# Performance work log

Measured on AMD Instinct MI355X. Metric: run time of the kernel, lower is better.

Reference implementation:

```python
import jax, jax.numpy as jnp
import numpy as np
import math

B, S, T = 8, 512, 512
D, H, DFF = 512, 8, 2048
LE, LD = 4, 4
DK = D // H
NEG = -1e9
EPS = 1e-5


def _posenc(L, d):
    pos = jnp.arange(L, dtype=jnp.float32)[:, None]
    div = jnp.exp(jnp.arange(0, d, 2, dtype=jnp.float32) * (-math.log(10000.0) / d))
    pe = jnp.zeros((L, d), jnp.float32)
    pe = pe.at[:, 0::2].set(jnp.sin(pos * div))
    pe = pe.at[:, 1::2].set(jnp.cos(pos * div))
    return pe  # [L, d]


def _layernorm(x, g, b):
    mu = jnp.mean(x, axis=-1, keepdims=True)
    var = jnp.mean(jnp.square(x - mu), axis=-1, keepdims=True)
    return (x - mu) * jax.lax.rsqrt(var + EPS) * g + b


def _mha(xq, xkv, W, b, mask):
    # W: [4, D, D] (q,k,v,o); b: [4, D]
    Bq, Lq, _ = xq.shape
    Lk = xkv.shape[1]
    q = (xq @ W[0] + b[0]).reshape(Bq, Lq, H, DK).transpose(0, 2, 1, 3)
    k = (xkv @ W[1] + b[1]).reshape(Bq, Lk, H, DK).transpose(0, 2, 1, 3)
    v = (xkv @ W[2] + b[2]).reshape(Bq, Lk, H, DK).transpose(0, 2, 1, 3)
    scores = jnp.einsum('bhqd,bhkd->bhqk', q, k) / math.sqrt(DK)
    if mask is not None:
        scores = jnp.where(mask, scores, NEG)
    attn = jax.nn.softmax(scores, axis=-1)
    o = jnp.einsum('bhqk,bhkd->bhqd', attn, v).transpose(0, 2, 1, 3).reshape(Bq, Lq, D)
    return o @ W[3] + b[3]


def _ffn(x, W1, b1, W2, b2):
    return jax.nn.relu(x @ W1 + b1) @ W2 + b2


def setup_inputs() -> dict:
    key = jax.random.key(0)
    ks = iter(jax.random.split(key, 32))
    w = lambda shape: jax.random.normal(next(ks), shape, jnp.float32) * 0.02
    inp = {
        'src': jax.random.normal(next(ks), (B, S, D), jnp.float32),
        'tgt': jax.random.normal(next(ks), (B, T, D), jnp.float32),
        'enc_attn_W': w((LE, 4, D, D)), 'enc_attn_b': jnp.zeros((LE, 4, D)),
        'enc_ffn_W1': w((LE, D, DFF)), 'enc_ffn_b1': jnp.zeros((LE, DFF)),
        'enc_ffn_W2': w((LE, DFF, D)), 'enc_ffn_b2': jnp.zeros((LE, D)),
        'enc_ln_g': jnp.ones((LE, 2, D)), 'enc_ln_b': jnp.zeros((LE, 2, D)),
        'enc_fnorm_g': jnp.ones((D,)), 'enc_fnorm_b': jnp.zeros((D,)),
        'dec_sattn_W': w((LD, 4, D, D)), 'dec_sattn_b': jnp.zeros((LD, 4, D)),
        'dec_cattn_W': w((LD, 4, D, D)), 'dec_cattn_b': jnp.zeros((LD, 4, D)),
        'dec_ffn_W1': w((LD, D, DFF)), 'dec_ffn_b1': jnp.zeros((LD, DFF)),
        'dec_ffn_W2': w((LD, DFF, D)), 'dec_ffn_b2': jnp.zeros((LD, D)),
        'dec_ln_g': jnp.ones((LD, 3, D)), 'dec_ln_b': jnp.zeros((LD, 3, D)),
        'dec_fnorm_g': jnp.ones((D,)), 'dec_fnorm_b': jnp.zeros((D,)),
        'tgt_mask': jnp.tril(jnp.ones((T, T), bool))[None, None],  # [1,1,T,T] causal
    }
    return inp


def reference(src, tgt, enc_attn_W, enc_attn_b, enc_ffn_W1, enc_ffn_b1,
              enc_ffn_W2, enc_ffn_b2, enc_ln_g, enc_ln_b, enc_fnorm_g, enc_fnorm_b,
              dec_sattn_W, dec_sattn_b, dec_cattn_W, dec_cattn_b,
              dec_ffn_W1, dec_ffn_b1, dec_ffn_W2, dec_ffn_b2,
              dec_ln_g, dec_ln_b, dec_fnorm_g, dec_fnorm_b, tgt_mask):
    # positional encoding (dropout = identity in eval)
    x = src + _posenc(S, D)[None]
    y = tgt + _posenc(T, D)[None]

    # ----- encoder -----
    for l in range(LE):
        a = _mha(x, x, enc_attn_W[l], enc_attn_b[l], None)
        x = _layernorm(x + a, enc_ln_g[l, 0], enc_ln_b[l, 0])
        f = _ffn(x, enc_ffn_W1[l], enc_ffn_b1[l], enc_ffn_W2[l], enc_ffn_b2[l])
        x = _layernorm(x + f, enc_ln_g[l, 1], enc_ln_b[l, 1])
    memory = _layernorm(x, enc_fnorm_g, enc_fnorm_b)

    # ----- decoder -----
    for l in range(LD):
        a = _mha(y, y, dec_sattn_W[l], dec_sattn_b[l], tgt_mask)
        y = _layernorm(y + a, dec_ln_g[l, 0], dec_ln_b[l, 0])
        c = _mha(y, memory, dec_cattn_W[l], dec_cattn_b[l], None)
        y = _layernorm(y + c, dec_ln_g[l, 1], dec_ln_b[l, 1])
        f = _ffn(y, dec_ffn_W1[l], dec_ffn_b1[l], dec_ffn_W2[l], dec_ffn_b2[l])
        y = _layernorm(y + f, dec_ln_g[l, 2], dec_ln_b[l, 2])
    out = _layernorm(y, dec_fnorm_g, dec_fnorm_b)
    return out
```

## Files before the change

kernel.cpp:

```cpp
#include <hip/hip_runtime.h>

typedef _Float16 half_t;
typedef _Float16 f16x8 __attribute__((ext_vector_type(8)));
typedef _Float16 f16x4 __attribute__((ext_vector_type(4)));
typedef float    f32x4 __attribute__((ext_vector_type(4)));

#define MFMA16(a, b, c) __builtin_amdgcn_mfma_f32_16x16x32_f16((a), (b), (c), 0, 0, 0)

#define BB   8
#define SS   512
#define DD   512
#define HH   8
#define DFFN 2048
#define MTOT 4096
#define MMAT 262144L
#define FFMAT 1048576L
#define ACTST 2097152L

__device__ __forceinline__ void gload16(const half_t* g, half_t* l) {
    __builtin_amdgcn_global_load_lds((const __attribute__((address_space(1))) void*)g,
                                     (__attribute__((address_space(3))) void*)l, 16, 0, 0);
}

__global__ __launch_bounds__(256) void wtrans(const float* __restrict__ W,
                                              half_t* __restrict__ Wt, int K, int N) {
    const long z = blockIdx.z;
    W += z * (long)K * N;
    Wt += z * (long)K * N;
    __shared__ float t[32][33];
    const int n0 = blockIdx.x * 32, k0 = blockIdx.y * 32;
    const int tx = threadIdx.x, ty = threadIdx.y;
#pragma unroll
    for (int i = 0; i < 4; i++)
        t[ty + i * 8][tx] = W[(long)(k0 + ty + i * 8) * N + n0 + tx];
    __syncthreads();
#pragma unroll
    for (int i = 0; i < 4; i++)
        Wt[(long)(n0 + ty + i * 8) * K + k0 + tx] = (half_t)t[tx][ty + i * 8];
}

__global__ __launch_bounds__(256) void vtrans(const half_t* __restrict__ V,
                                              half_t* __restrict__ Vt, int Lk) {
    const int z = blockIdx.z, b = z >> 3, h = z & 7;
    const int s0 = blockIdx.x * 32, d0 = blockIdx.y * 32;
    const int tx = threadIdx.x, ty = threadIdx.y;
    __shared__ half_t t[32][33];
#pragma unroll
    for (int i = 0; i < 4; i++)
        t[ty + i * 8][tx] = V[(long)(b * Lk + s0 + ty + i * 8) * DD + h * 64 + d0 + tx];
    __syncthreads();
#pragma unroll
    for (int i = 0; i < 4; i++)
        Vt[(long)(z * 64 + d0 + ty + i * 8) * Lk + s0 + tx] = t[tx][ty + i * 8];
}

__global__ __launch_bounds__(256) void vtransc(const half_t* __restrict__ ckv,
                                               half_t* __restrict__ vtc) {
    const int zz = blockIdx.z, l = zz >> 6, z = zz & 63, b = z >> 3, h = z & 7;
    const half_t* V = ckv + (long)(2 * l + 1) * ACTST;
    half_t* Vt = vtc + (long)l * ACTST;
    const int s0 = blockIdx.x * 32, d0 = blockIdx.y * 32;
    const int tx = threadIdx.x, ty = threadIdx.y;
    __shared__ half_t t[32][33];
#pragma unroll
    for (int i = 0; i < 4; i++)
        t[ty + i * 8][tx] = V[(long)(b * SS + s0 + ty + i * 8) * DD + h * 64 + d0 + tx];
    __syncthreads();
#pragma unroll
    for (int i = 0; i < 4; i++)
        Vt[(long)(z * 64 + d0 + ty + i * 8) * SS + s0 + tx] = t[tx][ty + i * 8];
}

__global__ __launch_bounds__(256) void posenc_k(const float* __restrict__ src,
                                                half_t* __restrict__ out) {
    const int idx = blockIdx.x * 256 + threadIdx.x;
    const long f = (long)idx * 4;
    const int d0 = (int)(f & 511);
    const int srow = (int)((f >> 9) & 511);
    float4 v = *(const float4*)(src + f);
    const float cexp = -0.0359778926f;
    const int p0 = d0 >> 1;
    const float a0 = (float)srow * __expf(cexp * (float)p0);
    const float a1 = (float)srow * __expf(cexp * (float)(p0 + 1));
    v.x += __sinf(a0);
    v.y += __cosf(a0);
    v.z += __sinf(a1);
    v.w += __cosf(a1);
    f16x4 h;
    h[0] = (half_t)v.x; h[1] = (half_t)v.y; h[2] = (half_t)v.z; h[3] = (half_t)v.w;
    *(f16x4*)(out + f) = h;
}

template <int HASRES, int F32OUT>
__global__ __launch_bounds__(256) void ln_k(const half_t* __restrict__ X,
                                            const half_t* __restrict__ R,
                                            const float* __restrict__ gam,
                                            const float* __restrict__ bet,
                                            void* __restrict__ out) {
    const int wid = threadIdx.x >> 6, lane = threadIdx.x & 63;
    const long row = blockIdx.x * 4 + wid;
    const int c = lane * 8;
    float v[8];
    f16x8 xv = *(const f16x8*)(X + row * 512 + c);
    if (HASRES) {
        f16x8 rv = *(const f16x8*)(R + row * 512 + c);
#pragma unroll
        for (int i = 0; i < 8; i++) v[i] = (float)xv[i] + (float)rv[i];
    } else {
#pragma unroll
        for (int i = 0; i < 8; i++) v[i] = (float)xv[i];
    }
    float s = 0.f, sq = 0.f;
#pragma unroll
    for (int i = 0; i < 8; i++) { s += v[i]; sq += v[i] * v[i]; }
#pragma unroll
    for (int m = 1; m < 64; m <<= 1) {
        s += __shfl_xor(s, m);
        sq += __shfl_xor(sq, m);
    }
    const float mu = s * (1.f / 512.f);
    const float var = sq * (1.f / 512.f) - mu * mu;
    const float rstd = rsqrtf(var + 1e-5f);
    float4 g0 = *(const float4*)(gam + c), g1 = *(const float4*)(gam + c + 4);
    float4 b0 = *(const float4*)(bet + c), b1 = *(const float4*)(bet + c + 4);
    float gg[8] = {g0.x, g0.y, g0.z, g0.w, g1.x, g1.y, g1.z, g1.w};
    float bb[8] = {b0.x, b0.y, b0.z, b0.w, b1.x, b1.y, b1.z, b1.w};
    if (F32OUT) {
        float* o = (float*)out + row * 512 + c;
        float4 o0, o1;
        o0.x = (v[0] - mu) * rstd * gg[0] + bb[0];
        o0.y = (v[1] - mu) * rstd * gg[1] + bb[1];
        o0.z = (v[2] - mu) * rstd * gg[2] + bb[2];
        o0.w = (v[3] - mu) * rstd * gg[3] + bb[3];
        o1.x = (v[4] - mu) * rstd * gg[4] + bb[4];
        o1.y = (v[5] - mu) * rstd * gg[5] + bb[5];
        o1.z = (v[6] - mu) * rstd * gg[6] + bb[6];
        o1.w = (v[7] - mu) * rstd * gg[7] + bb[7];
        *(float4*)o = o0;
        *(float4*)(o + 4) = o1;
    } else {
        f16x8 hv;
#pragma unroll
        for (int i = 0; i < 8; i++) hv[i] = (half_t)((v[i] - mu) * rstd * gg[i] + bb[i]);
        *(f16x8*)((half_t*)out + row * 512 + c) = hv;
    }
}

template <int MR, int RELU, int ZMAP>
__global__ __launch_bounds__(256) void gemm_k(const half_t* __restrict__ A,
                                              const half_t* __restrict__ Wt,
                                              const float* __restrict__ bias,
                                              half_t* __restrict__ C, int M, int N, int K,
                                              long wzs, long bzs, long czs) {
    constexpr int BM = MR * 32;
    __shared__ half_t smem[2][(BM + 64) * 64];
    const int z = blockIdx.z;
    const half_t* Wz;
    const float* bz;
    half_t* Cz;
    if (ZMAP) {
        const int l = z >> 1, i = z & 1;
        Wz = Wt + (long)(l * 4 + 1 + i) * MMAT;
        bz = bias + l * 2048 + (1 + i) * 512;
        Cz = C + (long)z * czs;
    } else {
        Wz = Wt + (long)z * wzs;
        bz = bias + (long)z * bzs;
        Cz = C + (long)z * czs;
    }
    const int m0 = blockIdx.x * BM, n0 = blockIdx.y * 64;
    const int tid = threadIdx.x, wid = tid >> 6, lane = tid & 63;
    const int g = lane >> 4, l16 = lane & 15;
    const int wr = wid >> 1, wc = wid & 1;
    const int nk = K >> 6;

    f32x4 acc[MR][2];
#pragma unroll
    for (int i = 0; i < MR; i++)
#pragma unroll
        for (int j = 0; j < 2; j++)
#pragma unroll
            for (int e = 0; e < 4; e++) acc[i][j][e] = 0.f;

    auto stage = [&](int buf, int kt) {
        half_t* sA = smem[buf];
        half_t* sB = smem[buf] + BM * 64;
        const int k0 = kt << 6;
#pragma unroll
        for (int i = 0; i < MR; i++) {
            const int c = i * 256 + wid * 64 + lane;
            const int r = c >> 3, j = c & 7, js = j ^ (r & 7);
            gload16(A + (long)(m0 + r) * K + k0 + js * 8, sA + (i * 256 + wid * 64) * 8);
        }
#pragma unroll
        for (int i = 0; i < 2; i++) {
            const int c = i * 256 + wid * 64 + lane;
            const int r = c >> 3, j = c & 7, js = j ^ (r & 7);
            gload16(Wz + (long)(n0 + r) * K + k0 + js * 8, sB + (i * 256 + wid * 64) * 8);
        }
    };

    stage(0, 0);
    __syncthreads();
    int buf = 0;
    for (int kt = 0; kt < nk; kt++) {
        if (kt + 1 < nk) stage(buf ^ 1, kt + 1);
        const half_t* sA = smem[buf];
        const half_t* sB = smem[buf] + BM * 64;
#pragma unroll
        for (int kk = 0; kk < 2; kk++) {
            f16x8 af[MR], bf[2];
#pragma unroll
            for (int mr = 0; mr < MR; mr++) {
                const int row = wr * (MR * 16) + mr * 16 + l16;
                af[mr] = *(const f16x8*)(sA + row * 64 + (((kk * 4 + g) ^ (row & 7)) * 8));
            }
#pragma unroll
            for (int nr = 0; nr < 2; nr++) {
                const int row = wc * 32 + nr * 16 + l16;
                bf[nr] = *(const f16x8*)(sB + row * 64 + (((kk * 4 + g) ^ (row & 7)) * 8));
            }
#pragma unroll
            for (int mr = 0; mr < MR; mr++)
#pragma unroll
                for (int nr = 0; nr < 2; nr++)
                    acc[mr][nr] = MFMA16(af[mr], bf[nr], acc[mr][nr]);
        }
        __syncthreads();
        buf ^= 1;
    }

#pragma unroll
    for (int nr = 0; nr < 2; nr++) {
        const int n = n0 + wc * 32 + nr * 16 + l16;
        const float bv = bz[n];
#pragma unroll
        for (int mr = 0; mr < MR; mr++) {
#pragma unroll
            for (int e = 0; e < 4; e++) {
                const int m = m0 + wr * (MR * 16) + mr * 16 + g * 4 + e;
                float v = acc[mr][nr][e] + bv;
                if (RELU) v = fmaxf(v, 0.f);
                Cz[(long)m * N + n] = (half_t)v;
            }
        }
    }
}

template <int CAUSAL>
__global__ __launch_bounds__(256) void flash_k(const half_t* __restrict__ Qb,
                                               const half_t* __restrict__ Kb,
                                               const half_t* __restrict__ Vt,
                                               half_t* __restrict__ Ob, int Lq, int Lk) {
    __shared__ half_t sQ[64 * 64];
    __shared__ half_t sK[2][64 * 64], sV[2][64 * 64];
    __shared__ half_t sP[4][16 * 88];
    const int qt = blockIdx.x, h = blockIdx.y, b = blockIdx.z;
    const int tid = threadIdx.x, wid = tid >> 6, lane = tid & 63;
    const int g = lane >> 4, l16 = lane & 15;

#pragma unroll
    for (int i = 0; i < 2; i++) {
        const int c = i * 256 + wid * 64 + lane;
        const int r = c >> 3, j = c & 7, js = j ^ (r & 7);
        gload16(Qb + (long)(b * Lq + qt * 64 + r) * DD + h * 64 + js * 8,
                sQ + (i * 256 + wid * 64) * 8);
    }
    auto stage_kv = [&](int bu, int kvt) {
#pragma unroll
        for (int i = 0; i < 2; i++) {
            const int c = i * 256 + wid * 64 + lane;
            const int r = c >> 3, j = c & 7, js = j ^ (r & 7);
            gload16(Kb + (long)(b * Lk + kvt * 64 + r) * DD + h * 64 + js * 8,
                    sK[bu] + (i * 256 + wid * 64) * 8);
            gload16(Vt + (long)((b * HH + h) * 64 + r) * Lk + kvt * 64 + js * 8,
                    sV[bu] + (i * 256 + wid * 64) * 8);
        }
    };

    float m_e[4], l_e[4];
#pragma unroll
    for (int e = 0; e < 4; e++) { m_e[e] = -1e30f; l_e[e] = 0.f; }
    f32x4 o[4];
#pragma unroll
    for (int d = 0; d < 4; d++)
#pragma unroll
        for (int e = 0; e < 4; e++) o[d][e] = 0.f;

    const int nkv = CAUSAL ? (qt + 1) : (Lk >> 6);
    stage_kv(0, 0);
    __syncthreads();
    int buf = 0;
    for (int kvt = 0; kvt < nkv; kvt++) {
        if (kvt + 1 < nkv) stage_kv(buf ^ 1, kvt + 1);
        const half_t* cK = sK[buf];
        const half_t* cV = sV[buf];

        f32x4 s[4];
#pragma unroll
        for (int nr = 0; nr < 4; nr++)
#pragma unroll
            for (int e = 0; e < 4; e++) s[nr][e] = 0.f;
#pragma unroll
        for (int k0 = 0; k0 < 2; k0++) {
            const int qrow = wid * 16 + l16;
            f16x8 aq = *(const f16x8*)(sQ + qrow * 64 + (((k0 * 4 + g) ^ (qrow & 7)) * 8));
#pragma unroll
            for (int nr = 0; nr < 4; nr++) {
                const int krow = nr * 16 + l16;
                f16x8 bk = *(const f16x8*)(cK + krow * 64 + (((k0 * 4 + g) ^ (krow & 7)) * 8));
                s[nr] = MFMA16(aq, bk, s[nr]);
            }
        }
        float mx[4];
#pragma unroll
        for (int e = 0; e < 4; e++) mx[e] = -1e30f;
#pragma unroll
        for (int nr = 0; nr < 4; nr++) {
#pragma unroll
            for (int e = 0; e < 4; e++) {
                float v = s[nr][e] * 0.125f;
                if (CAUSAL) {
                    const int q = qt * 64 + wid * 16 + g * 4 + e;
                    const int kv = kvt * 64 + nr * 16 + l16;
                    if (kv > q) v = -1e9f;
                }
                s[nr][e] = v;
                mx[e] = fmaxf(mx[e], v);
            }
        }
#pragma unroll
        for (int e = 0; e < 4; e++) {
            float v = mx[e];
            v = fmaxf(v, __shfl_xor(v, 1));
            v = fmaxf(v, __shfl_xor(v, 2));
            v = fmaxf(v, __shfl_xor(v, 4));
            v = fmaxf(v, __shfl_xor(v, 8));
            mx[e] = v;
        }
        float al[4], rs[4];
#pragma unroll
        for (int e = 0; e < 4; e++) {
            const float mn = fmaxf(m_e[e], mx[e]);
            al[e] = __expf(m_e[e] - mn);
            m_e[e] = mn;
            rs[e] = 0.f;
        }
#pragma unroll
        for (int nr = 0; nr < 4; nr++) {
#pragma unroll
            for (int e = 0; e < 4; e++) {
                const float p = __expf(s[nr][e] - m_e[e]);
                rs[e] += p;
                sP[wid][(g * 4 + e) * 88 + nr * 16 + l16] = (half_t)p;
            }
        }
#pragma unroll
        for (int e = 0; e < 4; e++) {
            float v = rs[e];
            v += __shfl_xor(v, 1);
            v += __shfl_xor(v, 2);
            v += __shfl_xor(v, 4);
            v += __shfl_xor(v, 8);
            l_e[e] = l_e[e] * al[e] + v;
        }
#pragma unroll
        for (int dr = 0; dr < 4; dr++)
#pragma unroll
            for (int e = 0; e < 4; e++) o[dr][e] *= al[e];
#pragma unroll
        for (int k0 = 0; k0 < 2; k0++) {
            f16x8 pa = *(const f16x8*)(&sP[wid][l16 * 88 + k0 * 32 + g * 8]);
#pragma unroll
            for (int dr = 0; dr < 4; dr++) {
                const int vrow = dr * 16 + l16;
                f16x8 vb = *(const f16x8*)(cV + vrow * 64 + (((k0 * 4 + g) ^ (vrow & 7)) * 8));
                o[dr] = MFMA16(pa, vb, o[dr]);
            }
        }
        __syncthreads();
        buf ^= 1;
    }
#pragma unroll
    for (int dr = 0; dr < 4; dr++) {
#pragma unroll
        for (int e = 0; e < 4; e++) {
            const int q = qt * 64 + wid * 16 + g * 4 + e;
            const int d = h * 64 + dr * 16 + l16;
            Ob[(long)(b * Lq + q) * DD + d] = (half_t)(o[dr][e] / l_e[e]);
        }
    }
}

static inline void launch_gemm(hipStream_t st, const half_t* A, const half_t* Wt,
                               const float* b, half_t* C, int M, int N, int K, int nz,
                               long wzs, long bzs, long czs, bool relu, int bm) {
    dim3 grid(M / bm, N / 64, nz), blk(256);
    if (bm == 128) {
        if (relu)
            gemm_k<4, 1, 0><<<grid, blk, 0, st>>>(A, Wt, b, C, M, N, K, wzs, bzs, czs);
        else
            gemm_k<4, 0, 0><<<grid, blk, 0, st>>>(A, Wt, b, C, M, N, K, wzs, bzs, czs);
    } else {
        if (relu)
            gemm_k<2, 1, 0><<<grid, blk, 0, st>>>(A, Wt, b, C, M, N, K, wzs, bzs, czs);
        else
            gemm_k<2, 0, 0><<<grid, blk, 0, st>>>(A, Wt, b, C, M, N, K, wzs, bzs, czs);
    }
}

extern "C" void kernel_launch(void* const* d_in, const int* in_sizes, int n_in, void* d_out,
                              int out_size, void* d_ws, size_t ws_size, hipStream_t stream) {
    (void)in_sizes; (void)n_in; (void)out_size; (void)ws_size;
    const float* src = (const float*)d_in[0];
    const float* tgt = (const float*)d_in[1];
    const float* eaW = (const float*)d_in[2];
    const float* eab = (const float*)d_in[3];
    const float* ef1W = (const float*)d_in[4];
    const float* ef1b = (const float*)d_in[5];
    const float* ef2W = (const float*)d_in[6];
    const float* ef2b = (const float*)d_in[7];
    const float* elng = (const float*)d_in[8];
    const float* elnb = (const float*)d_in[9];
    const float* efng = (const float*)d_in[10];
    const float* efnb = (const float*)d_in[11];
    const float* dsW = (const float*)d_in[12];
    const float* dsb = (const float*)d_in[13];
    const float* dcW = (const float*)d_in[14];
    const float* dcb = (const float*)d_in[15];
    const float* df1W = (const float*)d_in[16];
    const float* df1b = (const float*)d_in[17];
    const float* df2W = (const float*)d_in[18];
    const float* df2b = (const float*)d_in[19];
    const float* dlng = (const float*)d_in[20];
    const float* dlnb = (const float*)d_in[21];
    const float* dfng = (const float*)d_in[22];
    const float* dfnb = (const float*)d_in[23];

    char* ws = (char*)d_ws;
    half_t* wtEA = (half_t*)(ws + 0);
    half_t* wtEF1 = (half_t*)(ws + 8388608);
    half_t* wtEF2 = (half_t*)(ws + 16777216);
    half_t* wtDS = (half_t*)(ws + 25165824);
    half_t* wtDC = (half_t*)(ws + 33554432);
    half_t* wtDF1 = (half_t*)(ws + 41943040);
    half_t* wtDF2 = (half_t*)(ws + 50331648);
    half_t* xb = (half_t*)(ws + 58720256);
    half_t* yb = (half_t*)(ws + 62914560);
    half_t* memb = (half_t*)(ws + 67108864);
    half_t* qb = (half_t*)(ws + 71303168);
    half_t* kb = (half_t*)(ws + 75497472);
    half_t* vb = (half_t*)(ws + 79691776);
    half_t* vtb = (half_t*)(ws + 83886080);
    half_t* ao = (half_t*)(ws + 88080384);
    half_t* pr = (half_t*)(ws + 92274688);
    half_t* ffh = (half_t*)(ws + 96468992);
    half_t* ff2 = (half_t*)(ws + 113246208);
    half_t* ckv = (half_t*)(ws + 134217728);
    half_t* vtc = (half_t*)(ws + 167772160);

    dim3 tb(32, 8);
    wtrans<<<dim3(16, 16, 16), tb, 0, stream>>>(eaW, wtEA, 512, 512);
    wtrans<<<dim3(64, 16, 4), tb, 0, stream>>>(ef1W, wtEF1, 512, 2048);
    wtrans<<<dim3(16, 64, 4), tb, 0, stream>>>(ef2W, wtEF2, 2048, 512);
    wtrans<<<dim3(16, 16, 16), tb, 0, stream>>>(dsW, wtDS, 512, 512);
    wtrans<<<dim3(16, 16, 16), tb, 0, stream>>>(dcW, wtDC, 512, 512);
    wtrans<<<dim3(64, 16, 4), tb, 0, stream>>>(df1W, wtDF1, 512, 2048);
    wtrans<<<dim3(16, 64, 4), tb, 0, stream>>>(df2W, wtDF2, 2048, 512);

    posenc_k<<<2048, 256, 0, stream>>>(src, xb);
    posenc_k<<<2048, 256, 0, stream>>>(tgt, yb);

    for (int l = 0; l < 4; l++) {
        launch_gemm(stream, xb, wtEA + (long)l * 4 * MMAT, eab + l * 2048, qb, MTOT, 512, 512,
                    3, MMAT, 512, ACTST, false, 128);
        vtrans<<<dim3(16, 2, 64), tb, 0, stream>>>(vb, vtb, 512);
        flash_k<0><<<dim3(8, 8, 8), 256, 0, stream>>>(qb, kb, vtb, ao, 512, 512);
        launch_gemm(stream, ao, wtEA + (long)(l * 4 + 3) * MMAT, eab + l * 2048 + 1536, pr,
                    MTOT, 512, 512, 1, 0, 0, 0, false, 64);
        ln_k<1, 0><<<1024, 256, 0, stream>>>(pr, xb, elng + l * 1024, elnb + l * 1024, xb);
        launch_gemm(stream, xb, wtEF1 + (long)l * FFMAT, ef1b + l * 2048, ffh, MTOT, 2048,
                    512, 1, 0, 0, 0, true, 128);
        launch_gemm(stream, ffh, wtEF2 + (long)l * FFMAT, ef2b + l * 512, ff2, MTOT, 512,
                    2048, 1, 0, 0, 0, false, 64);
        ln_k<1, 0><<<1024, 256, 0, stream>>>(ff2, xb, elng + l * 1024 + 512,
                                             elnb + l * 1024 + 512, xb);
    }
    ln_k<0, 0><<<1024, 256, 0, stream>>>(xb, nullptr, efng, efnb, memb);

    gemm_k<4, 0, 1><<<dim3(32, 8, 8), 256, 0, stream>>>(memb, wtDC, dcb, ckv, MTOT, 512,
                                                        512, 0, 0, ACTST);
    vtransc<<<dim3(16, 2, 256), tb, 0, stream>>>(ckv, vtc);

    for (int l = 0; l < 4; l++) {
        launch_gemm(stream, yb, wtDS + (long)l * 4 * MMAT, dsb + l * 2048, qb, MTOT, 512, 512,
                    3, MMAT, 512, ACTST, false, 128);
        vtrans<<<dim3(16, 2, 64), tb, 0, stream>>>(vb, vtb, 512);
        flash_k<1><<<dim3(8, 8, 8), 256, 0, stream>>>(qb, kb, vtb, ao, 512, 512);
        launch_gemm(stream, ao, wtDS + (long)(l * 4 + 3) * MMAT, dsb + l * 2048 + 1536, pr,
                    MTOT, 512, 512, 1, 0, 0, 0, false, 64);
        ln_k<1, 0><<<1024, 256, 0, stream>>>(pr, yb, dlng + l * 1536, dlnb + l * 1536, yb);
        launch_gemm(stream, yb, wtDC + (long)l * 4 * MMAT, dcb + l * 2048, qb, MTOT, 512, 512,
                    1, 0, 0, 0, false, 64);
        flash_k<0><<<dim3(8, 8, 8), 256, 0, stream>>>(qb, ckv + (long)(2 * l) * ACTST,
                                                      vtc + (long)l * ACTST, ao, 512, 512);
        launch_gemm(stream, ao, wtDC + (long)(l * 4 + 3) * MMAT, dcb + l * 2048 + 1536, pr,
                    MTOT, 512, 512, 1, 0, 0, 0, false, 64);
        ln_k<1, 0><<<1024, 256, 0, stream>>>(pr, yb, dlng + l * 1536 + 512,
                                             dlnb + l * 1536 + 512, yb);
        launch_gemm(stream, yb, wtDF1 + (long)l * FFMAT, df1b + l * 2048, ffh, MTOT, 2048,
                    512, 1, 0, 0, 0, true, 128);
        launch_gemm(stream, ffh, wtDF2 + (long)l * FFMAT, df2b + l * 512, ff2, MTOT, 512,
                    2048, 1, 0, 0, 0, false, 64);
        ln_k<1, 0><<<1024, 256, 0, stream>>>(ff2, yb, dlng + l * 1536 + 1024,
                                             dlnb + l * 1536 + 1024, yb);
    }
    ln_k<0, 1><<<1024, 256, 0, stream>>>(yb, nullptr, dfng, dfnb, d_out);
}
```

Before: 1.083 ms.

## Triple-buffer GEMM loads and use vmcnt-based waits instead of full syncthreads

```diff
diff --git a/kernel.cpp b/kernel.cpp
--- a/kernel.cpp
+++ b/kernel.cpp
@@ -16,6 +16,9 @@
 #define MMAT 262144L
 #define FFMAT 1048576L
 #define ACTST 2097152L
+
+#define WAITV(n) asm volatile("s_waitcnt vmcnt(" #n ")" ::: "memory")
+#define SBAR()   asm volatile("s_barrier" ::: "memory")
 
 __device__ __forceinline__ void gload16(const half_t* g, half_t* l) {
     __builtin_amdgcn_global_load_lds((const __attribute__((address_space(1))) void*)g,
@@ -153,7 +156,7 @@
                                               half_t* __restrict__ C, int M, int N, int K,
                                               long wzs, long bzs, long czs) {
     constexpr int BM = MR * 32;
-    __shared__ half_t smem[2][(BM + 64) * 64];
+    __shared__ half_t smem[3][(BM + 64) * 64];
     const int z = blockIdx.z;
     const half_t* Wz;
     const float* bz;
@@ -182,9 +185,9 @@
 #pragma unroll
             for (int e = 0; e < 4; e++) acc[i][j][e] = 0.f;
 
-    auto stage = [&](int buf, int kt) {
-        half_t* sA = smem[buf];
-        half_t* sB = smem[buf] + BM * 64;
+    auto stage = [&](int s, int kt) {
+        half_t* sA = smem[s];
+        half_t* sB = smem[s] + BM * 64;
         const int k0 = kt << 6;
 #pragma unroll
         for (int i = 0; i < MR; i++) {
@@ -201,12 +204,21 @@
     };
 
     stage(0, 0);
-    __syncthreads();
-    int buf = 0;
+    if (nk > 1) stage(1, 1);
     for (int kt = 0; kt < nk; kt++) {
-        if (kt + 1 < nk) stage(buf ^ 1, kt + 1);
-        const half_t* sA = smem[buf];
-        const half_t* sB = smem[buf] + BM * 64;
+        if (kt + 2 < nk) stage((kt + 2) % 3, kt + 2);
+        if constexpr (MR == 4) {
+            if (kt + 2 < nk) WAITV(12);
+            else if (kt + 1 < nk) WAITV(6);
+            else WAITV(0);
+        } else {
+            if (kt + 2 < nk) WAITV(8);
+            else if (kt + 1 < nk) WAITV(4);
+            else WAITV(0);
+        }
+        SBAR();
+        const half_t* sA = smem[kt % 3];
+        const half_t* sB = smem[kt % 3] + BM * 64;
 #pragma unroll
         for (int kk = 0; kk < 2; kk++) {
             f16x8 af[MR], bf[2];
@@ -226,8 +238,7 @@
                 for (int nr = 0; nr < 2; nr++)
                     acc[mr][nr] = MFMA16(af[mr], bf[nr], acc[mr][nr]);
         }
-        __syncthreads();
-        buf ^= 1;
+        SBAR();
     }
 
 #pragma unroll
@@ -289,10 +300,15 @@
 
     const int nkv = CAUSAL ? (qt + 1) : (Lk >> 6);
     stage_kv(0, 0);
-    __syncthreads();
     int buf = 0;
     for (int kvt = 0; kvt < nkv; kvt++) {
-        if (kvt + 1 < nkv) stage_kv(buf ^ 1, kvt + 1);
+        if (kvt + 1 < nkv) {
+            stage_kv(buf ^ 1, kvt + 1);
+            WAITV(4);
+        } else {
+            WAITV(0);
+        }
+        SBAR();
         const half_t* cK = sK[buf];
         const half_t* cV = sV[buf];
 
@@ -378,7 +394,7 @@
                 o[dr] = MFMA16(pa, vb, o[dr]);
             }
         }
-        __syncthreads();
+        SBAR();
         buf ^= 1;
     }
 #pragma unroll
```

Result: faster. 1.058 ms (-2.3%).
